# Kernel optimization log

Measured on AMD Instinct MI355X. Metric: run time of the kernel, lower is better.

## Reference

```python
import jax, jax.numpy as jnp
import numpy as np

B, S, D_MODEL, D_MEM, N_HEADS, NU = 8, 2048, 1024, 1024, 16, 3
D_HEAD = D_MODEL // N_HEADS            # 64
D_KEY = 2 * NU * (D_MEM // N_HEADS)    # 384


def _to_heads(x, n_heads):
    b, s, d = x.shape
    return x.reshape(b, s, n_heads, d // n_heads).transpose(0, 2, 1, 3)


def _dpfp(x, nu):
    # Deterministic Positive Feature Projection: (..., d) -> (..., 2*nu*d)
    x = jnp.concatenate([jax.nn.relu(x), jax.nn.relu(-x)], axis=-1)
    rolled = jnp.concatenate([jnp.roll(x, j, axis=-1) for j in range(1, nu + 1)], axis=-1)
    rep = jnp.concatenate([x] * nu, axis=-1)
    return rep * rolled


def setup_inputs() -> dict:
    key = jax.random.key(0)
    k0, k1, k2, k3, k4 = jax.random.split(key, 5)
    mem_tokens = jax.random.normal(k0, (B, S, D_MODEL), dtype=jnp.float32)
    # nn.Linear(in, out) weight shape is [out, in]
    W_mk = jax.random.normal(k1, (D_MEM, D_MODEL), dtype=jnp.float32) * 0.02
    W_mv = jax.random.normal(k2, (D_MODEL, D_MODEL), dtype=jnp.float32) * 0.02
    W_mb = jax.random.normal(k3, (D_MODEL, D_MODEL), dtype=jnp.float32) * 0.02
    W_mem = jax.random.normal(k4, (B, N_HEADS, D_KEY, D_HEAD), dtype=jnp.float32) * 0.01
    z = jnp.ones((B, N_HEADS, D_KEY), dtype=jnp.float32)
    return {"mem_tokens": mem_tokens, "W_mk": W_mk, "W_mv": W_mv, "W_mb": W_mb,
            "W_mem": W_mem, "z": z}


def reference(mem_tokens, W_mk, W_mv, W_mb, W_mem, z):
    # key projection + DPFP feature map
    k = _to_heads(mem_tokens @ W_mk.T, N_HEADS)          # [b,h,s,d_mem/h]
    mk = _dpfp(k, NU)                                     # [b,h,s,d_key]
    norm = jnp.linalg.norm(mk, axis=-1, keepdims=True)
    mk = mk / jnp.maximum(norm, 1e-12)                    # F.normalize(p=2)

    new_mv = _to_heads(mem_tokens @ W_mv.T, N_HEADS)      # [b,h,s,d_head]

    # retrieve previous values (first_seg=False, use_denom=True path)
    num = jnp.einsum('bhsk,bhkd->bhsd', mk, W_mem)
    denom = jnp.einsum('bhk,bhsk->bhs', z, mk)[..., None] + 1e-5
    prev_mv = num / denom

    mv = new_mv - prev_mv
    mb = _to_heads(jax.nn.sigmoid(mem_tokens @ W_mb.T), N_HEADS)

    # gating=True einsum: 'ihjk,ihjt,ihjt->ihkt'
    associations = jnp.einsum('bhsk,bhsd,bhsd->bhkd', mk, mv, mb)
    return W_mem + associations
```

## Files before the change

kernel.cpp:

```cpp
#include <hip/hip_runtime.h>
#include <hip/hip_bf16.h>

#define B_ 8
#define S_ 2048
#define DM 1024
#define H_ 16
#define DH 64
#define DK 384

#define AS3 __attribute__((address_space(3)))
#define AS1 __attribute__((address_space(1)))
typedef unsigned int u32;

typedef __attribute__((ext_vector_type(8))) short bf16x8;
typedef __attribute__((ext_vector_type(4))) short bf16x4;
typedef __attribute__((ext_vector_type(4))) float f32x4;

static __device__ __forceinline__ ushort f2b(float f) {
  __hip_bfloat16 h = __float2bfloat16(f);
  return *reinterpret_cast<ushort*>(&h);
}
static __device__ __forceinline__ float b2f(ushort u) {
  __hip_bfloat16 h;
  *reinterpret_cast<ushort*>(&h) = u;
  return __bfloat162float(h);
}

__global__ __launch_bounds__(256) void k_cvt(
    const float* __restrict__ X, const float* __restrict__ Wk,
    const float* __restrict__ Wv, const float* __restrict__ Wb,
    ushort* __restrict__ Xb, ushort* __restrict__ Wball) {
  const int total = 2097152 + 3 * 131072;
  int c = blockIdx.x * 256 + threadIdx.x;
  const int stride = gridDim.x * 256;
  for (; c < total; c += stride) {
    const float* s;
    ushort* d;
    size_t off;
    if (c < 2097152) { s = X; d = Xb; off = (size_t)c; }
    else {
      int cc = c - 2097152;
      int wsel = cc >> 17;
      off = (size_t)(cc & 131071);
      s = wsel == 0 ? Wk : (wsel == 1 ? Wv : Wb);
      d = Wball + (size_t)wsel * (DM * DM);
    }
    float4 a = *(const float4*)(s + off * 8);
    float4 b = *(const float4*)(s + off * 8 + 4);
    ushort u[8] = { f2b(a.x), f2b(a.y), f2b(a.z), f2b(a.w),
                    f2b(b.x), f2b(b.y), f2b(b.z), f2b(b.w) };
    *(uint4*)(d + off * 8) = *(uint4*)u;
  }
}

__global__ __launch_bounds__(512) void k_proj(
    const ushort* __restrict__ Xb, const ushort* __restrict__ Wball,
    ushort* __restrict__ kvb) {
  __shared__ ushort SH[3 * 24576];
  const int t = threadIdx.x, lane = t & 63, w = t >> 6;
  const int wm = w >> 1, wn = w & 1;
  const int l15 = lane & 15, lq = lane >> 4;
  const int bid = blockIdx.x + (blockIdx.y << 6) + (blockIdx.z << 9);
  const int c = bid & 7, r = bid >> 3;
  const int zb = r >> 6;
  const int rem = r & 63;
  const int mgrp = rem >> 3;
  const int nb = rem & 7;
  const int m0 = (c * 8 + mgrp) * 256;
  const int n0 = nb * 128;
  const int wsel = zb;
  const ushort* Wmat = Wball + (size_t)wsel * (DM * DM);
  ushort* out = kvb + (size_t)wsel * ((size_t)B_ * H_ * S_ * DH);

  const int srow = t >> 3;
  const int scol8 = ((t & 7) ^ (srow & 7)) * 8;

  const ushort* pA[4];
  const ushort* pB[2];
  #pragma unroll
  for (int j = 0; j < 4; j++)
    pA[j] = Xb + (size_t)(m0 + j * 64 + srow) * DM + scol8;
  #pragma unroll
  for (int j = 0; j < 2; j++)
    pB[j] = Wmat + (size_t)(n0 + j * 64 + srow) * DM + scol8;

  auto STAGE = [&](int buf, int kidx) {
    ushort* base = SH + buf * 24576;
    #pragma unroll
    for (int j = 0; j < 4; j++)
      __builtin_amdgcn_global_load_lds(
          (const AS1 u32*)(pA[j] + kidx * 64),
          (AS3 u32*)(base + j * 4096 + t * 8), 16, 0, 0);
    #pragma unroll
    for (int j = 0; j < 2; j++)
      __builtin_amdgcn_global_load_lds(
          (const AS1 u32*)(pB[j] + kidx * 64),
          (AS3 u32*)(base + 16384 + j * 4096 + t * 8), 16, 0, 0);
  };

  const int aoffb = (wm * 64 + l15) * 64;
  const int boffb = 16384 + (wn * 64 + l15) * 64;
  const int csw0 = (lq ^ (lane & 7)) << 3;
  const int csw1 = ((lq + 4) ^ (lane & 7)) << 3;

  f32x4 acc[4][4] = {};
  STAGE(0, 0);
  STAGE(1, 1);
  #pragma unroll
  for (int kt = 0; kt < 16; kt++) {
    if (kt < 15) asm volatile("s_waitcnt vmcnt(6)" ::: "memory");
    else         asm volatile("s_waitcnt vmcnt(0)" ::: "memory");
    __builtin_amdgcn_s_barrier();
    if (kt < 14) STAGE((kt + 2) % 3, kt + 2);
    const ushort* Ab = SH + (kt % 3) * 24576;
    __builtin_amdgcn_s_setprio(1);
    #pragma unroll
    for (int kk2 = 0; kk2 < 2; kk2++) {
      const int csw = kk2 ? csw1 : csw0;
      bf16x8 af[4], bfr[4];
      #pragma unroll
      for (int mi = 0; mi < 4; mi++)
        af[mi] = *(const bf16x8*)&Ab[aoffb + mi * 1024 + csw];
      #pragma unroll
      for (int ni = 0; ni < 4; ni++)
        bfr[ni] = *(const bf16x8*)&Ab[boffb + ni * 1024 + csw];
      #pragma unroll
      for (int mi = 0; mi < 4; mi++)
        #pragma unroll
        for (int ni = 0; ni < 4; ni++)
          acc[mi][ni] = __builtin_amdgcn_mfma_f32_16x16x32_bf16(af[mi], bfr[ni], acc[mi][ni], 0, 0, 0);
    }
    __builtin_amdgcn_s_setprio(0);
  }
  __syncthreads();

  ushort (*Cb)[136] = (ushort (*)[136])SH;
  #pragma unroll
  for (int mi = 0; mi < 4; mi++)
    #pragma unroll
    for (int ni = 0; ni < 4; ni++)
      #pragma unroll
      for (int rr = 0; rr < 4; rr++) {
        float val = acc[mi][ni][rr];
        if (wsel == 2) val = 1.0f / (1.0f + __expf(-val));
        Cb[wm * 64 + mi * 16 + lq * 4 + rr][wn * 64 + ni * 16 + l15] = f2b(val);
      }
  __syncthreads();
  #pragma unroll
  for (int q = 0; q < 8; q++) {
    int idx = q * 512 + t;
    int lm = idx >> 4;
    int c16 = idx & 15;
    int m = m0 + lm;
    int b = m >> 11, s = m & 2047;
    int o0 = n0 + c16 * 8;
    int h = o0 >> 6, d = o0 & 63;
    *(uint4*)(out + (((size_t)(b * H_ + h)) * S_ + s) * DH + d) =
        *(uint4*)&Cb[lm][c16 * 8];
  }
}

__global__ __launch_bounds__(512) void k_fused6(
    const ushort* __restrict__ Kb, const ushort* __restrict__ Vb,
    const ushort* __restrict__ Bgb, const float* __restrict__ Wmem,
    const float* __restrict__ z, ushort* __restrict__ part) {
  __shared__ u32 mkLd[32][192];
  __shared__ ushort mkT[384][36];
  __shared__ ushort gLT[64][36];
  __shared__ ushort zL[384];
  const int t = threadIdx.x, l = t & 63, w = t >> 6;
  const int l15 = l & 15, lq = l >> 4;
  const int bh = blockIdx.y, seg = blockIdx.x;
  const size_t rowbase = (size_t)bh * S_;
  const int mi = w >> 2, ni = w & 3;
  const int dcol = ni * 16 + l15;

  for (int cc = t; cc < DK; cc += 512) {
    int u = cc >> 7, p = (cc & 127) >> 1, par = cc & 1;
    zL[cc] = f2b(z[(size_t)bh * DK + u * 128 + par * 64 + p]);
  }

  const float* Wm = Wmem + (size_t)bh * (DK * DH);
  bf16x8 bw[12];
  #pragma unroll
  for (int k0i = 0; k0i < 12; k0i++) {
    bf16x8 tmp;
    #pragma unroll
    for (int j = 0; j < 8; j++) {
      int cc = k0i * 32 + lq * 8 + j;
      int u = cc >> 7, p = (cc & 127) >> 1, par = cc & 1;
      tmp[j] = (short)f2b(Wm[(size_t)(u * 128 + par * 64 + p) * DH + dcol]);
    }
    bw[k0i] = tmp;
  }

  f32x4 acc[3][4] = {};
  ushort kreg[4], vreg[4], breg[4];

  auto LOADCH = [&](int ch) {
    const int s0 = seg * 512 + ch * 32;
    #pragma unroll
    for (int r = 0; r < 4; r++)
      kreg[r] = Kb[(rowbase + s0 + w * 4 + r) * DH + l];
    #pragma unroll
    for (int rr = 0; rr < 4; rr++) {
      size_t ga = (rowbase + s0 + mi * 16 + lq * 4 + rr) * DH + dcol;
      vreg[rr] = Vb[ga];
      breg[rr] = Bgb[ga];
    }
  };

  LOADCH(0);
  __syncthreads();

  for (int ch = 0; ch < 16; ch++) {
    float xpv[4], xnv[4];
    u32 pks[4];
    #pragma unroll
    for (int r = 0; r < 4; r++) {
      float kv = b2f(kreg[r]);
      xpv[r] = fmaxf(kv, 0.f);
      xnv[r] = fmaxf(-kv, 0.f);
      pks[r] = (u32)f2b(xpv[r]) | ((u32)f2b(xnv[r]) << 16);
    }
    ushort4 mp[6];
    #pragma unroll
    for (int u = 0; u < 3; u++) {
      int ie = (l - u - 1) & 127;
      int sl = ie & 63;
      bool sw = ie >= 64;
      #pragma unroll
      for (int r = 0; r < 4; r++) {
        u32 pp = (u32)__shfl((int)pks[r], sl);
        float ps = b2f((ushort)(pp & 0xffff));
        float ns = b2f((ushort)(pp >> 16));
        float xbe = sw ? ns : ps;
        float xbo = sw ? ps : ns;
        ushort bve = f2b(xpv[r] * xbe);
        ushort bvo = f2b(xnv[r] * xbo);
        int row = w * 4 + r;
        mkLd[row][(u * 64 + l) ^ ((row & 7) << 2)] = (u32)bve | ((u32)bvo << 16);
        ((ushort*)&mp[2 * u])[r] = bve;
        ((ushort*)&mp[2 * u + 1])[r] = bvo;
      }
    }
    #pragma unroll
    for (int tt = 0; tt < 6; tt++)
      *(ushort4*)&mkT[l + 64 * tt][w * 4] = mp[tt];
    __syncthreads();

    const u32* mkrow = &mkLd[mi * 16 + l15][0];
    const int xr = (l15 & 7) << 2;
    f32x4 an0 = {}, an1 = {}, gacc = {}, zacc = {};
    __builtin_amdgcn_s_setprio(1);
    #pragma unroll
    for (int k0i = 0; k0i < 12; k0i += 2) {
      bf16x8 afA = *(const bf16x8*)(mkrow + ((k0i * 16 + lq * 4) ^ xr));
      bf16x8 afB = *(const bf16x8*)(mkrow + (((k0i + 1) * 16 + lq * 4) ^ xr));
      bf16x8 zfA = *(const bf16x8*)&zL[k0i * 32 + lq * 8];
      bf16x8 zfB = *(const bf16x8*)&zL[(k0i + 1) * 32 + lq * 8];
      an0 = __builtin_amdgcn_mfma_f32_16x16x32_bf16(afA, bw[k0i], an0, 0, 0, 0);
      an1 = __builtin_amdgcn_mfma_f32_16x16x32_bf16(afB, bw[k0i + 1], an1, 0, 0, 0);
      gacc = __builtin_amdgcn_mfma_f32_16x16x32_bf16(afA, afA, gacc, 0, 0, 0);
      gacc = __builtin_amdgcn_mfma_f32_16x16x32_bf16(afB, afB, gacc, 0, 0, 0);
      zacc = __builtin_amdgcn_mfma_f32_16x16x32_bf16(afA, zfA, zacc, 0, 0, 0);
      zacc = __builtin_amdgcn_mfma_f32_16x16x32_bf16(afB, zfB, zacc, 0, 0, 0);
    }
    __builtin_amdgcn_s_setprio(0);
    f32x4 an = an0 + an1;
    float ssqv[4];
    #pragma unroll
    for (int rr = 0; rr < 4; rr++)
      ssqv[rr] = __shfl(gacc[rr], (lq << 4) + lq * 4 + rr);
    {
      ushort4 gp;
      #pragma unroll
      for (int rr = 0; rr < 4; rr++) {
        float inv = 1.0f / fmaxf(sqrtf(ssqv[rr]), 1e-12f);
        float rden = 1.0f / (inv * zacc[rr] + 1e-5f);
        float prev = an[rr] * inv * rden;
        float g = (b2f(vreg[rr]) - prev) * b2f(breg[rr]);
        ((ushort*)&gp)[rr] = f2b(g * inv);
      }
      *(ushort4*)&gLT[dcol][mi * 16 + lq * 4] = gp;
    }
    __syncthreads();

    if (ch < 15) LOADCH(ch + 1);

    {
      bf16x8 bfr[4];
      #pragma unroll
      for (int n2 = 0; n2 < 4; n2++) {
        bf16x4 blo = *(const bf16x4*)&gLT[n2 * 16 + l15][lq * 8];
        bf16x4 bhi = *(const bf16x4*)&gLT[n2 * 16 + l15][lq * 8 + 4];
        bfr[n2] = __builtin_shufflevector(blo, bhi, 0, 1, 2, 3, 4, 5, 6, 7);
      }
      __builtin_amdgcn_s_setprio(1);
      #pragma unroll
      for (int m2 = 0; m2 < 3; m2++) {
        bf16x4 alo = *(const bf16x4*)&mkT[w * 48 + m2 * 16 + l15][lq * 8];
        bf16x4 ahi = *(const bf16x4*)&mkT[w * 48 + m2 * 16 + l15][lq * 8 + 4];
        bf16x8 af = __builtin_shufflevector(alo, ahi, 0, 1, 2, 3, 4, 5, 6, 7);
        #pragma unroll
        for (int n2 = 0; n2 < 4; n2++)
          acc[m2][n2] = __builtin_amdgcn_mfma_f32_16x16x32_bf16(af, bfr[n2], acc[m2][n2], 0, 0, 0);
      }
      __builtin_amdgcn_s_setprio(0);
    }
    __syncthreads();
  }

  ushort* pb = part + ((size_t)bh * 4 + seg) * (DK * DH);
  #pragma unroll
  for (int m2 = 0; m2 < 3; m2++)
    #pragma unroll
    for (int n2 = 0; n2 < 4; n2++)
      #pragma unroll
      for (int rc = 0; rc < 4; rc++)
        pb[(size_t)(w * 48 + m2 * 16 + lq * 4 + rc) * DH + n2 * 16 + l15] =
            f2b(acc[m2][n2][rc]);
}

__global__ __launch_bounds__(256) void k_reduce(
    const float* __restrict__ Wmem, const ushort* __restrict__ part,
    float* __restrict__ out) {
  size_t i4 = (size_t)blockIdx.x * 256 + threadIdx.x;
  int bh = (int)(i4 / 6144);
  size_t r4 = i4 - (size_t)bh * 6144;
  float4 acc = *(const float4*)(Wmem + i4 * 4);
  #pragma unroll
  for (int k = 0; k < 4; k++) {
    const ushort* pp = part + ((size_t)bh * 4 + k) * (DK * DH) + r4 * 4;
    ushort4 pv = *(const ushort4*)pp;
    acc.x += b2f(pv.x);
    acc.y += b2f(pv.y);
    acc.z += b2f(pv.z);
    acc.w += b2f(pv.w);
  }
  *(float4*)(out + i4 * 4) = acc;
}

extern "C" void kernel_launch(void* const* d_in, const int* in_sizes, int n_in,
                              void* d_out, int out_size, void* d_ws, size_t ws_size,
                              hipStream_t stream) {
  const float* X  = (const float*)d_in[0];
  const float* Wk = (const float*)d_in[1];
  const float* Wv = (const float*)d_in[2];
  const float* Wb = (const float*)d_in[3];
  const float* Wm = (const float*)d_in[4];
  const float* z  = (const float*)d_in[5];
  float* out = (float*)d_out;
  char* ws = (char*)d_ws;

  ushort* Xb    = (ushort*)(ws);
  ushort* Wball = (ushort*)(ws + 33554432ull);
  ushort* kvb   = (ushort*)(ws + 39845888ull);
  ushort* part  = (ushort*)(ws);
  ushort* Kb  = kvb;
  ushort* Vb  = kvb + (size_t)B_ * H_ * S_ * DH;
  ushort* Bgb = kvb + 2ull * (size_t)B_ * H_ * S_ * DH;

  k_cvt   <<<dim3(2048), 256, 0, stream>>>(X, Wk, Wv, Wb, Xb, Wball);
  k_proj  <<<dim3(64, 8, 3), 512, 0, stream>>>(Xb, Wball, kvb);
  k_fused6<<<dim3(4, B_ * H_), 512, 0, stream>>>(Kb, Vb, Bgb, Wm, z, part);
  k_reduce<<<dim3(3072), 256, 0, stream>>>(Wm, part, out);
}
```

Measured before the change: 239.6 us.

## Enlarge projection GEMM tile to 256x256 with BK=32 and split epilogue

The projection GEMM block tile grows from 256x128 to 256x256, with the K step cut from 64 to 32 so the triple-buffered LDS footprint shrinks. Warps are rearranged as 2x4, each computing a 128x64 sub-tile (8x4 MFMA accumulators). The LDS swizzle is reworked for the 32-wide K slices, and the epilogue writes out in two 128-row halves through LDS. The aim is more operand reuse and fewer global loads per MFMA. The cost is more accumulator registers per thread, half as many blocks, and twice as many barrier-separated K iterations.

```diff
diff --git a/kernel.cpp b/kernel.cpp
--- a/kernel.cpp
+++ b/kernel.cpp
@@ -56,107 +56,107 @@
 __global__ __launch_bounds__(512) void k_proj(
     const ushort* __restrict__ Xb, const ushort* __restrict__ Wball,
     ushort* __restrict__ kvb) {
-  __shared__ ushort SH[3 * 24576];
+  __shared__ ushort SH[3 * 16384];
   const int t = threadIdx.x, lane = t & 63, w = t >> 6;
-  const int wm = w >> 1, wn = w & 1;
+  const int wm = w >> 2, wn = w & 3;
   const int l15 = lane & 15, lq = lane >> 4;
-  const int bid = blockIdx.x + (blockIdx.y << 6) + (blockIdx.z << 9);
+  const int bid = blockIdx.x + (blockIdx.y << 6) + (blockIdx.z << 8);
   const int c = bid & 7, r = bid >> 3;
-  const int zb = r >> 6;
-  const int rem = r & 63;
-  const int mgrp = rem >> 3;
-  const int nb = rem & 7;
+  const int zb = r >> 5;
+  const int rem = r & 31;
+  const int mgrp = rem >> 2;
+  const int nb = rem & 3;
   const int m0 = (c * 8 + mgrp) * 256;
-  const int n0 = nb * 128;
+  const int n0 = nb * 256;
   const int wsel = zb;
   const ushort* Wmat = Wball + (size_t)wsel * (DM * DM);
   ushort* out = kvb + (size_t)wsel * ((size_t)B_ * H_ * S_ * DH);
 
-  const int srow = t >> 3;
-  const int scol8 = ((t & 7) ^ (srow & 7)) * 8;
-
-  const ushort* pA[4];
+  const int chk = t >> 6;
+  const int ql = t & 63;
+  const int srow = ql >> 2;
+  const int scol8 = ((ql & 3) ^ ((ql >> 3) & 3)) * 8;
+
+  const ushort* pA[2];
   const ushort* pB[2];
   #pragma unroll
-  for (int j = 0; j < 4; j++)
-    pA[j] = Xb + (size_t)(m0 + j * 64 + srow) * DM + scol8;
-  #pragma unroll
-  for (int j = 0; j < 2; j++)
-    pB[j] = Wmat + (size_t)(n0 + j * 64 + srow) * DM + scol8;
+  for (int j = 0; j < 2; j++) {
+    pA[j] = Xb + (size_t)(m0 + j * 128 + chk * 16 + srow) * DM + scol8;
+    pB[j] = Wmat + (size_t)(n0 + j * 128 + chk * 16 + srow) * DM + scol8;
+  }
 
   auto STAGE = [&](int buf, int kidx) {
-    ushort* base = SH + buf * 24576;
-    #pragma unroll
-    for (int j = 0; j < 4; j++)
-      __builtin_amdgcn_global_load_lds(
-          (const AS1 u32*)(pA[j] + kidx * 64),
-          (AS3 u32*)(base + j * 4096 + t * 8), 16, 0, 0);
+    ushort* base = SH + buf * 16384;
     #pragma unroll
     for (int j = 0; j < 2; j++)
       __builtin_amdgcn_global_load_lds(
-          (const AS1 u32*)(pB[j] + kidx * 64),
-          (AS3 u32*)(base + 16384 + j * 4096 + t * 8), 16, 0, 0);
+          (const AS1 u32*)(pA[j] + kidx * 32),
+          (AS3 u32*)(base + j * 4096 + t * 8), 16, 0, 0);
+    #pragma unroll
+    for (int j = 0; j < 2; j++)
+      __builtin_amdgcn_global_load_lds(
+          (const AS1 u32*)(pB[j] + kidx * 32),
+          (AS3 u32*)(base + 8192 + j * 4096 + t * 8), 16, 0, 0);
   };
 
-  const int aoffb = (wm * 64 + l15) * 64;
-  const int boffb = 16384 + (wn * 64 + l15) * 64;
-  const int csw0 = (lq ^ (lane & 7)) << 3;
-  const int csw1 = ((lq + 4) ^ (lane & 7)) << 3;
-
-  f32x4 acc[4][4] = {};
+  const int rofs = (l15 * 4 + (lq ^ ((l15 >> 1) & 3))) * 8;
+
+  f32x4 acc[8][4] = {};
   STAGE(0, 0);
   STAGE(1, 1);
   #pragma unroll
-  for (int kt = 0; kt < 16; kt++) {
-    if (kt < 15) asm volatile("s_waitcnt vmcnt(6)" ::: "memory");
+  for (int kt = 0; kt < 32; kt++) {
+    if (kt < 31) asm volatile("s_waitcnt vmcnt(4)" ::: "memory");
     else         asm volatile("s_waitcnt vmcnt(0)" ::: "memory");
     __builtin_amdgcn_s_barrier();
-    if (kt < 14) STAGE((kt + 2) % 3, kt + 2);
-    const ushort* Ab = SH + (kt % 3) * 24576;
+    if (kt < 30) STAGE((kt + 2) % 3, kt + 2);
+    const ushort* Ab = SH + (kt % 3) * 16384;
     __builtin_amdgcn_s_setprio(1);
-    #pragma unroll
-    for (int kk2 = 0; kk2 < 2; kk2++) {
-      const int csw = kk2 ? csw1 : csw0;
-      bf16x8 af[4], bfr[4];
-      #pragma unroll
-      for (int mi = 0; mi < 4; mi++)
-        af[mi] = *(const bf16x8*)&Ab[aoffb + mi * 1024 + csw];
+    bf16x8 af[8], bfr[4];
+    #pragma unroll
+    for (int mi = 0; mi < 8; mi++)
+      af[mi] = *(const bf16x8*)&Ab[(wm * 8 + mi) * 512 + rofs];
+    #pragma unroll
+    for (int ni = 0; ni < 4; ni++)
+      bfr[ni] = *(const bf16x8*)&Ab[8192 + (wn * 4 + ni) * 512 + rofs];
+    #pragma unroll
+    for (int mi = 0; mi < 8; mi++)
       #pragma unroll
       for (int ni = 0; ni < 4; ni++)
-        bfr[ni] = *(const bf16x8*)&Ab[boffb + ni * 1024 + csw];
-      #pragma unroll
-      for (int mi = 0; mi < 4; mi++)
+        acc[mi][ni] = __builtin_amdgcn_mfma_f32_16x16x32_bf16(af[mi], bfr[ni], acc[mi][ni], 0, 0, 0);
+    __builtin_amdgcn_s_setprio(0);
+  }
+  __syncthreads();
+
+  ushort (*Cb)[264] = (ushort (*)[264])SH;
+  #pragma unroll
+  for (int hf = 0; hf < 2; hf++) {
+    if (wm == hf) {
+      #pragma unroll
+      for (int mi = 0; mi < 8; mi++)
         #pragma unroll
         for (int ni = 0; ni < 4; ni++)
-          acc[mi][ni] = __builtin_amdgcn_mfma_f32_16x16x32_bf16(af[mi], bfr[ni], acc[mi][ni], 0, 0, 0);
-    }
-    __builtin_amdgcn_s_setprio(0);
-  }
-  __syncthreads();
-
-  ushort (*Cb)[136] = (ushort (*)[136])SH;
-  #pragma unroll
-  for (int mi = 0; mi < 4; mi++)
-    #pragma unroll
-    for (int ni = 0; ni < 4; ni++)
-      #pragma unroll
-      for (int rr = 0; rr < 4; rr++) {
-        float val = acc[mi][ni][rr];
-        if (wsel == 2) val = 1.0f / (1.0f + __expf(-val));
-        Cb[wm * 64 + mi * 16 + lq * 4 + rr][wn * 64 + ni * 16 + l15] = f2b(val);
-      }
-  __syncthreads();
-  #pragma unroll
-  for (int q = 0; q < 8; q++) {
-    int idx = q * 512 + t;
-    int lm = idx >> 4;
-    int c16 = idx & 15;
-    int m = m0 + lm;
-    int b = m >> 11, s = m & 2047;
-    int o0 = n0 + c16 * 8;
-    int h = o0 >> 6, d = o0 & 63;
-    *(uint4*)(out + (((size_t)(b * H_ + h)) * S_ + s) * DH + d) =
-        *(uint4*)&Cb[lm][c16 * 8];
+          #pragma unroll
+          for (int rr = 0; rr < 4; rr++) {
+            float val = acc[mi][ni][rr];
+            if (wsel == 2) val = 1.0f / (1.0f + __expf(-val));
+            Cb[mi * 16 + lq * 4 + rr][wn * 64 + ni * 16 + l15] = f2b(val);
+          }
+    }
+    __syncthreads();
+    #pragma unroll
+    for (int q = 0; q < 8; q++) {
+      int idx = q * 512 + t;
+      int lm = idx >> 5;
+      int c16 = idx & 31;
+      int m = m0 + hf * 128 + lm;
+      int b = m >> 11, s = m & 2047;
+      int o0 = n0 + c16 * 8;
+      int h = o0 >> 6, d = o0 & 63;
+      *(uint4*)(out + (((size_t)(b * H_ + h)) * S_ + s) * DH + d) =
+          *(uint4*)&Cb[lm][c16 * 8];
+    }
+    __syncthreads();
   }
 }
 
@@ -362,7 +362,7 @@
   ushort* Bgb = kvb + 2ull * (size_t)B_ * H_ * S_ * DH;
 
   k_cvt   <<<dim3(2048), 256, 0, stream>>>(X, Wk, Wv, Wb, Xb, Wball);
-  k_proj  <<<dim3(64, 8, 3), 512, 0, stream>>>(Xb, Wball, kvb);
+  k_proj  <<<dim3(64, 4, 3), 512, 0, stream>>>(Xb, Wball, kvb);
   k_fused6<<<dim3(4, B_ * H_), 512, 0, stream>>>(Kb, Vb, Bgb, Wm, z, part);
   k_reduce<<<dim3(3072), 256, 0, stream>>>(Wm, part, out);
 }
```

After: 241.8 us. About the same (+0.9%).
